# Performance work log

Measured on AMD Instinct MI355X. Metric: run time of the kernel, lower is better.

## Reference

```python
import jax, jax.numpy as jnp
import numpy as np

B, T, S, D, H = 8, 512, 512, 512, 8
DH = D // H
EPS = 1e-5


def _ln(x, g, b):
    m = x.mean(-1, keepdims=True)
    v = x.var(-1, keepdims=True)
    return (x - m) / jnp.sqrt(v + EPS) * g + b


def setup_inputs() -> dict:
    key = jax.random.key(0)
    ks = jax.random.split(key, 24)
    w = lambda k, shp: (jax.random.normal(k, shp, jnp.float32) * 0.02)
    causal = jnp.where(jnp.tril(jnp.ones((T, T), bool)), 0.0, -1e9).astype(jnp.float32)
    return {
        "tgt": jax.random.normal(ks[0], (B, T, D), jnp.float32),
        "memory": jax.random.normal(ks[1], (B, S, D), jnp.float32),
        "tgt_mask": causal,
        "gate": jax.random.uniform(ks[2], (T, D), jnp.float32),
        # self-attn params (torch MultiheadAttention packed in_proj layout)
        "sa_in_w": w(ks[3], (3 * D, D)), "sa_in_b": w(ks[4], (3 * D,)),
        "sa_out_w": w(ks[5], (D, D)), "sa_out_b": w(ks[6], (D,)),
        # cross-attn params
        "ca_in_w": w(ks[7], (3 * D, D)), "ca_in_b": w(ks[8], (3 * D,)),
        "ca_out_w": w(ks[9], (D, D)), "ca_out_b": w(ks[10], (D,)),
        # FFN
        "ff1_w": w(ks[11], (4 * D, D)), "ff1_b": w(ks[12], (4 * D,)),
        "ff2_w": w(ks[13], (D, 4 * D)), "ff2_b": w(ks[14], (D,)),
        # layernorms
        "ln1_g": jnp.ones((D,), jnp.float32), "ln1_b": jnp.zeros((D,), jnp.float32),
        "ln2_g": jnp.ones((D,), jnp.float32), "ln2_b": jnp.zeros((D,), jnp.float32),
        "ln3_g": jnp.ones((D,), jnp.float32), "ln3_b": jnp.zeros((D,), jnp.float32),
    }


def reference(tgt, memory, tgt_mask, gate,
              sa_in_w, sa_in_b, sa_out_w, sa_out_b,
              ca_in_w, ca_in_b, ca_out_w, ca_out_b,
              ff1_w, ff1_b, ff2_w, ff2_b,
              ln1_g, ln1_b, ln2_g, ln2_b, ln3_g, ln3_b):
    b, t, d = tgt.shape
    s = memory.shape[1]
    scale = 1.0 / jnp.sqrt(jnp.float32(DH))

    # ---- self attention (standard batched MHA, additive mask) ----
    wq, wk, wv = jnp.split(sa_in_w, 3, axis=0)
    bq, bk, bv = jnp.split(sa_in_b, 3, axis=0)
    q = ((tgt @ wq.T + bq).reshape(b, t, H, DH)) * scale
    k = (tgt @ wk.T + bk).reshape(b, t, H, DH)
    v = (tgt @ wv.T + bv).reshape(b, t, H, DH)
    scores = jnp.einsum('bthd,bshd->bhts', q, k) + tgt_mask  # (B,H,T,T)
    attn = jax.nn.softmax(scores, axis=-1)
    sa = jnp.einsum('bhts,bshd->bthd', attn, v).reshape(b, t, d) @ sa_out_w.T + sa_out_b
    x = _ln(tgt + sa, ln1_g, ln1_b)

    # ---- gated cross attention ----
    # Original: key_{b,t,s} = W_k(gate_t * memory_{b,s}) + b_k materialized as (B*T,S,D).
    # Faithful refactor: distribute W_k, fold (q W_k) with gate into the query side.
    cwq, cwk, cwv = jnp.split(ca_in_w, 3, axis=0)
    cbq, cbk, cbv = jnp.split(ca_in_b, 3, axis=0)
    cq = ((x @ cwq.T + cbq).reshape(b, t, H, DH)) * scale          # (B,T,H,dh)
    wk_h = cwk.reshape(H, DH, d)                                    # (H,dh,D)
    qW = jnp.einsum('bthe,hed->bthd', cq, wk_h)                     # (B,T,H,D)
    cscores = jnp.einsum('bthd,td,bsd->bhts', qW, gate, memory)     # (B,H,T,S)
    bk_h = cbk.reshape(H, DH)
    cscores = cscores + jnp.einsum('bthe,he->bht', cq, bk_h)[..., None]
    cattn = jax.nn.softmax(cscores, axis=-1)
    cv = (memory @ cwv.T + cbv).reshape(b, s, H, DH)
    ca = jnp.einsum('bhts,bshe->bthe', cattn, cv).reshape(b, t, d) @ ca_out_w.T + ca_out_b
    x = _ln(x + ca, ln2_g, ln2_b)

    # ---- FFN ----
    ff = jax.nn.relu(x @ ff1_w.T + ff1_b) @ ff2_w.T + ff2_b
    return _ln(x + ff, ln3_g, ln3_b)
```

## Files before the change

kernel.cpp:

```cpp
#include <hip/hip_runtime.h>
#include <hip/hip_bf16.h>

#define BB 8
#define TT 512
#define SS 512
#define DD 512
#define HH 8

typedef __attribute__((ext_vector_type(8))) short bf16x8;
typedef __attribute__((ext_vector_type(4))) float f32x4;
typedef unsigned short u16;

__device__ __forceinline__ u16 f2b(float f) {
    __hip_bfloat16 h = __float2bfloat16(f);
    return *reinterpret_cast<u16*>(&h);
}
__device__ __forceinline__ float b2f(u16 v) {
    unsigned int u = ((unsigned int)v) << 16;
    return __builtin_bit_cast(float, u);
}
__device__ __forceinline__ void g2lds16(const void* g, void* l) {
    __builtin_amdgcn_global_load_lds(
        (const __attribute__((address_space(1))) void*)g,
        (__attribute__((address_space(3))) void*)l, 16, 0, 0);
}
template <int N> __device__ __forceinline__ void waitvm();
template <> __device__ __forceinline__ void waitvm<0>()  { asm volatile("s_waitcnt vmcnt(0)" ::: "memory"); }
template <> __device__ __forceinline__ void waitvm<4>()  { asm volatile("s_waitcnt vmcnt(4)" ::: "memory"); }
template <> __device__ __forceinline__ void waitvm<6>()  { asm volatile("s_waitcnt vmcnt(6)" ::: "memory"); }
template <> __device__ __forceinline__ void waitvm<8>()  { asm volatile("s_waitcnt vmcnt(8)" ::: "memory"); }
__device__ __forceinline__ void barrier_raw() {
    asm volatile("" ::: "memory");
    __builtin_amdgcn_s_barrier();
    asm volatile("" ::: "memory");
}
__device__ __forceinline__ void xcd_swz(int& bx, int& by, int& bz) {
    const int gx = gridDim.x, gy = gridDim.y, gz = gridDim.z;
    const int n = gx * gy * gz;
    const int flat = bx + gx * (by + gy * bz);
    const int q = n >> 3;
    const int nf = (flat & 7) * q + (flat >> 3);
    bx = nf % gx;
    const int r = nf / gx;
    by = r % gy;
    bz = r / gy;
}

struct CastSegs {
    const float* s[9];
    u16* d[9];
    int cum[10];
    const float* wsrc;
    u16* wdst;
};
__global__ __launch_bounds__(256) void cast_multi(CastSegs sg) {
    const int total = sg.cum[9];
    for (int i = blockIdx.x * 256 + threadIdx.x; i < total; i += gridDim.x * 256) {
        int k = 0;
#pragma unroll
        for (int j = 1; j < 9; ++j) k += (i >= sg.cum[j]);
        const int loc = i - sg.cum[k];
        float4 v = ((const float4*)sg.s[k])[loc];
        ushort4 u;
        u.x = f2b(v.x); u.y = f2b(v.y); u.z = f2b(v.z); u.w = f2b(v.w);
        ((ushort4*)sg.d[k])[loc] = u;
    }
    for (int idx = blockIdx.x * 256 + threadIdx.x; idx < 262144; idx += gridDim.x * 256) {
        const int h = idx >> 15, d = (idx >> 6) & 511, e = idx & 63;
        sg.wdst[idx] = f2b(sg.wsrc[(size_t)(512 + h * 64 + e) * 512 + d]);
    }
}

template <int TM, int TN, bool RELU, bool GATE, typename OutT = u16, bool ADDBIAS = true>
__global__ __launch_bounds__(256) void gemm_bf16(
    const u16* __restrict__ A, int lda, long az,
    const u16* __restrict__ Bw, int ldb, long bz,
    const float* __restrict__ bias, const float* __restrict__ biasB,
    const float* __restrict__ gate,
    OutT* __restrict__ C, int ldo, long cz,
    int K, float alpha, float alphaB) {
    __shared__ __align__(16) u16 As[2][TM * 64];
    __shared__ __align__(16) u16 Bs[2][TN * 64];
    int bx = blockIdx.x, by = blockIdx.y, bzz = blockIdx.z;
    xcd_swz(bx, by, bzz);
    const int tid = threadIdx.x;
    const int wave = tid >> 6, lane = tid & 63;
    const int lm = lane & 15, lg = lane >> 4;
    const int wm = wave >> 1, wn = wave & 1;
    const int m0 = by * TM, n0 = bx * TN;
    A += (size_t)bzz * az;
    Bw += (size_t)bzz * bz;
    C += (size_t)bzz * cz;
    constexpr int MI = TM / 32;
    constexpr int FN = TN / 32;
    constexpr int LPS = MI + FN;

    f32x4 acc[MI][FN];
#pragma unroll
    for (int mi = 0; mi < MI; ++mi)
#pragma unroll
        for (int ni = 0; ni < FN; ++ni) acc[mi][ni] = (f32x4){0.f, 0.f, 0.f, 0.f};

    const int srow = lane >> 3;
    const int sbyte = ((lane & 7) << 4) ^ (srow << 4);
    const int xk = (lm & 7) << 4;

    auto stage = [&](int buf, int kt) {
#pragma unroll
        for (int j = 0; j < MI; ++j) {
            const int r = wave * (TM / 4) + j * 8;
            g2lds16((const char*)(A + (size_t)(m0 + r + srow) * lda + kt) + sbyte,
                    (char*)As[buf] + (size_t)r * 128);
        }
#pragma unroll
        for (int j = 0; j < FN; ++j) {
            const int r = wave * (TN / 4) + j * 8;
            g2lds16((const char*)(Bw + (size_t)(n0 + r + srow) * ldb + kt) + sbyte,
                    (char*)Bs[buf] + (size_t)r * 128);
        }
    };

    stage(0, 0);
    const int NK = K >> 6;
    for (int t = 0; t < NK; ++t) {
        const int cur = t & 1;
        if (t + 1 < NK) { stage(cur ^ 1, (t + 1) << 6); waitvm<LPS>(); }
        else            { waitvm<0>(); }
        barrier_raw();
#pragma unroll
        for (int kh = 0; kh < 2; ++kh) {
            const int cb = kh * 64 + lg * 16;
            bf16x8 af[MI], bfr[FN];
#pragma unroll
            for (int mi = 0; mi < MI; ++mi) {
                const int row = wm * (TM / 2) + mi * 16 + lm;
                af[mi] = *(const bf16x8*)((const char*)As[cur] + row * 128 + (cb ^ xk));
            }
#pragma unroll
            for (int ni = 0; ni < FN; ++ni) {
                const int row = wn * (TN / 2) + ni * 16 + lm;
                bfr[ni] = *(const bf16x8*)((const char*)Bs[cur] + row * 128 + (cb ^ xk));
            }
#pragma unroll
            for (int mi = 0; mi < MI; ++mi)
#pragma unroll
                for (int ni = 0; ni < FN; ++ni)
                    acc[mi][ni] = __builtin_amdgcn_mfma_f32_16x16x32_bf16(
                        af[mi], bfr[ni], acc[mi][ni], 0, 0, 0);
        }
        barrier_raw();
    }

    const float* bp = bzz ? biasB : bias;
    const float al = bzz ? alphaB : alpha;
#pragma unroll
    for (int mi = 0; mi < MI; ++mi)
#pragma unroll
        for (int ni = 0; ni < FN; ++ni)
#pragma unroll
            for (int r = 0; r < 4; ++r) {
                const int m = m0 + wm * (TM / 2) + mi * 16 + lg * 4 + r;
                const int n = n0 + wn * (TN / 2) + ni * 16 + lm;
                float v = acc[mi][ni][r];
                if constexpr (GATE) v *= gate[(size_t)(m & 511) * 512 + n];
                else if constexpr (ADDBIAS) v = (v + bp[n]) * al;
                if constexpr (RELU) v = fmaxf(v, 0.f);
                if constexpr (sizeof(OutT) == 2) C[(size_t)m * ldo + n] = (OutT)f2b(v);
                else                             C[(size_t)m * ldo + n] = v;
            }
}

__global__ __launch_bounds__(256) void gemm_scores(
    const u16* __restrict__ QWp, const u16* __restrict__ membp,
    u16* __restrict__ SC) {
    __shared__ __align__(16) u16 As[2][128 * 64];
    __shared__ __align__(16) u16 Bs[2][64 * 64];
    int bx = blockIdx.x, by = blockIdx.y, bzz = blockIdx.z;
    xcd_swz(bx, by, bzz);
    const int tid = threadIdx.x;
    const int wave = tid >> 6, lane = tid & 63;
    const int lm = lane & 15, lg = lane >> 4;
    const int wm = wave >> 1, wn = wave & 1;
    const int m0 = by * 128, n0 = bx * 64;
    const int z = bzz, b = z >> 3, h = z & 7;
    const u16* A  = QWp + (size_t)b * TT * 4096 + h * 512;
    const u16* Bw = membp + (size_t)b * SS * 512;
    u16* C = SC + ((size_t)z << 18);

    f32x4 acc[4][2];
#pragma unroll
    for (int mi = 0; mi < 4; ++mi)
#pragma unroll
        for (int ni = 0; ni < 2; ++ni) acc[mi][ni] = (f32x4){0.f, 0.f, 0.f, 0.f};

    const int srow = lane >> 3;
    const int sbyte = ((lane & 7) << 4) ^ (srow << 4);
    const int xk = (lm & 7) << 4;

    auto stage = [&](int buf, int kt) {
#pragma unroll
        for (int j = 0; j < 4; ++j) {
            const int r = wave * 32 + j * 8;
            g2lds16((const char*)(A + (size_t)(m0 + r + srow) * 4096 + kt) + sbyte,
                    (char*)As[buf] + (size_t)r * 128);
        }
#pragma unroll
        for (int j = 0; j < 2; ++j) {
            const int r = wave * 16 + j * 8;
            g2lds16((const char*)(Bw + (size_t)(n0 + r + srow) * 512 + kt) + sbyte,
                    (char*)Bs[buf] + (size_t)r * 128);
        }
    };

    stage(0, 0);
    for (int t = 0; t < 8; ++t) {
        const int cur = t & 1;
        if (t + 1 < 8) { stage(cur ^ 1, (t + 1) << 6); waitvm<6>(); }
        else           { waitvm<0>(); }
        barrier_raw();
#pragma unroll
        for (int kh = 0; kh < 2; ++kh) {
            const int cb = kh * 64 + lg * 16;
            bf16x8 af[4], bfr[2];
#pragma unroll
            for (int mi = 0; mi < 4; ++mi) {
                const int row = wm * 64 + mi * 16 + lm;
                af[mi] = *(const bf16x8*)((const char*)As[cur] + row * 128 + (cb ^ xk));
            }
#pragma unroll
            for (int ni = 0; ni < 2; ++ni) {
                const int row = wn * 32 + ni * 16 + lm;
                bfr[ni] = *(const bf16x8*)((const char*)Bs[cur] + row * 128 + (cb ^ xk));
            }
#pragma unroll
            for (int mi = 0; mi < 4; ++mi)
#pragma unroll
                for (int ni = 0; ni < 2; ++ni)
                    acc[mi][ni] = __builtin_amdgcn_mfma_f32_16x16x32_bf16(
                        af[mi], bfr[ni], acc[mi][ni], 0, 0, 0);
        }
        barrier_raw();
    }
#pragma unroll
    for (int mi = 0; mi < 4; ++mi)
#pragma unroll
        for (int ni = 0; ni < 2; ++ni)
#pragma unroll
            for (int r = 0; r < 4; ++r) {
                const int m = m0 + wm * 64 + mi * 16 + lg * 4 + r;
                const int n = n0 + wn * 32 + ni * 16 + lm;
                C[(size_t)m * 512 + n] = f2b(acc[mi][ni][r]);
            }
}

__global__ __launch_bounds__(256) void softmax_pv(
    const u16* __restrict__ SC, const u16* __restrict__ CV,
    u16* __restrict__ out) {
    int btx = blockIdx.x, bh = blockIdx.y, bb = blockIdx.z;
    xcd_swz(btx, bh, bb);
    const int t0 = btx * 64, h = bh, b = bb;
    const int tid = threadIdx.x, wave = tid >> 6, lane = tid & 63;
    const int lm = lane & 15, lg = lane >> 4;
    __shared__ __align__(16) u16 Vt[64 * 512];

    {
        const int sp = tid * 2;
#pragma unroll
        for (int c = 0; c < 8; ++c) {
            bf16x8 v0 = *(const bf16x8*)(CV + ((size_t)b * SS + sp) * 512 + h * 64 + c * 8);
            bf16x8 v1 = *(const bf16x8*)(CV + ((size_t)b * SS + sp + 1) * 512 + h * 64 + c * 8);
#pragma unroll
            for (int j = 0; j < 8; ++j) {
                const int d = c * 8 + j;
                const unsigned int pk = (unsigned int)(u16)v0[j] |
                                        ((unsigned int)(u16)v1[j] << 16);
                *(unsigned int*)((char*)Vt + ((d << 10) + ((sp * 2) ^ ((d & 7) << 4)))) = pk;
            }
        }
    }

    const int tw = t0 + wave * 16;
    const u16* srow = SC + ((size_t)(b * 8 + h) << 18) + (size_t)(tw + lm) * 512 + lg * 8;
    float sa[16][8];
#pragma unroll
    for (int k = 0; k < 16; ++k) {
        const bf16x8 sv = *(const bf16x8*)(srow + k * 32);
#pragma unroll
        for (int j = 0; j < 8; ++j) sa[k][j] = b2f((u16)sv[j]);
    }
    float mx = -3e38f;
#pragma unroll
    for (int k = 0; k < 16; ++k)
#pragma unroll
        for (int j = 0; j < 8; ++j) mx = fmaxf(mx, sa[k][j]);
    mx = fmaxf(mx, __shfl_xor(mx, 16));
    mx = fmaxf(mx, __shfl_xor(mx, 32));
    float sum = 0.f;
    bf16x8 pb[16];
#pragma unroll
    for (int k = 0; k < 16; ++k) {
#pragma unroll
        for (int j = 0; j < 8; ++j) {
            const float p = __expf(sa[k][j] - mx);
            sum += p;
            pb[k][j] = (short)f2b(p);
        }
    }
    sum += __shfl_xor(sum, 16);
    sum += __shfl_xor(sum, 32);

    __syncthreads();

    f32x4 o[4];
#pragma unroll
    for (int nt = 0; nt < 4; ++nt) o[nt] = (f32x4){0.f, 0.f, 0.f, 0.f};
#pragma unroll
    for (int k = 0; k < 16; ++k) {
#pragma unroll
        for (int nt = 0; nt < 4; ++nt) {
            const int d = nt * 16 + lm;
            const bf16x8 vf = *(const bf16x8*)((const char*)Vt +
                ((d << 10) + ((k * 64 + lg * 16) ^ ((d & 7) << 4))));
            o[nt] = __builtin_amdgcn_mfma_f32_16x16x32_bf16(pb[k], vf, o[nt], 0, 0, 0);
        }
    }
#pragma unroll
    for (int r = 0; r < 4; ++r) {
        const float rs = __shfl(sum, lg * 4 + r);
        const float inv = 1.f / rs;
#pragma unroll
        for (int nt = 0; nt < 4; ++nt)
            out[(size_t)(b * TT + tw + lg * 4 + r) * DD + h * 64 + nt * 16 + lm] =
                f2b(o[nt][r] * inv);
    }
}

__global__ __launch_bounds__(256) void flash_self(const u16* __restrict__ QKV,
                                                  u16* __restrict__ out) {
    int btx = blockIdx.x, bh = blockIdx.y, bb = blockIdx.z;
    xcd_swz(btx, bh, bb);
    const int t0 = btx * 64, h = bh, b = bb;
    const int tid = threadIdx.x, wave = tid >> 6, lane = tid & 63;
    const int lm = lane & 15, lg = lane >> 4;
    __shared__ __align__(16) u16 Ks[32 * 64];
    __shared__ __align__(16) u16 Vt[64][40];
    __shared__ __align__(16) u16 P[4][16][40];

    const int tw = t0 + wave * 16;
    const size_t qrow = (size_t)(b * TT + tw + lm) * 1536 + h * 64;
    bf16x8 qf[2];
    qf[0] = *(const bf16x8*)(QKV + qrow + lg * 8);
    qf[1] = *(const bf16x8*)(QKV + qrow + 32 + lg * 8);

    float m_run[4], l_run[4];
    f32x4 oacc[4];
#pragma unroll
    for (int r = 0; r < 4; ++r) { m_run[r] = -3e38f; l_run[r] = 0.f; }
#pragma unroll
    for (int nt = 0; nt < 4; ++nt) oacc[nt] = (f32x4){0.f, 0.f, 0.f, 0.f};

    const int srow = lane >> 3, sbyte = ((lane & 7) << 4) ^ (srow << 4);
    const int xk = (lm & 7) << 4;
    const int smax = t0 + 64;
    for (int s0 = 0; s0 < smax; s0 += 32) {
        if (s0) __syncthreads();
        g2lds16((const char*)(QKV + (size_t)(b * TT + s0 + wave * 8 + srow) * 1536 +
                              512 + h * 64) + sbyte,
                (char*)Ks + wave * 1024);
        {
            const int s = tid & 31, d0 = (tid >> 5) * 8;
            bf16x8 vv = *(const bf16x8*)(QKV + (size_t)(b * TT + s0 + s) * 1536 +
                                         1024 + h * 64 + d0);
#pragma unroll
            for (int j = 0; j < 8; ++j) Vt[d0 + j][s] = (u16)vv[j];
        }
        __syncthreads();
        if (s0 <= tw + 15) {
            f32x4 sc0 = (f32x4){0.f, 0.f, 0.f, 0.f};
            f32x4 sc1 = (f32x4){0.f, 0.f, 0.f, 0.f};
#pragma unroll
            for (int f = 0; f < 2; ++f) {
                const int cb = f * 64 + lg * 16;
                bf16x8 k0 = *(const bf16x8*)((const char*)Ks + lm * 128 + (cb ^ xk));
                bf16x8 k1 = *(const bf16x8*)((const char*)Ks + (16 + lm) * 128 + (cb ^ xk));
                sc0 = __builtin_amdgcn_mfma_f32_16x16x32_bf16(qf[f], k0, sc0, 0, 0, 0);
                sc1 = __builtin_amdgcn_mfma_f32_16x16x32_bf16(qf[f], k1, sc1, 0, 0, 0);
            }
            float sv0[4], sv1[4], tm[4];
#pragma unroll
            for (int r = 0; r < 4; ++r) {
                const int t = tw + lg * 4 + r;
                sv0[r] = sc0[r] * 0.125f + ((s0 + lm) <= t ? 0.f : -1e9f);
                sv1[r] = sc1[r] * 0.125f + ((s0 + 16 + lm) <= t ? 0.f : -1e9f);
                tm[r] = fmaxf(sv0[r], sv1[r]);
            }
#pragma unroll
            for (int off = 1; off < 16; off <<= 1)
#pragma unroll
                for (int r = 0; r < 4; ++r) tm[r] = fmaxf(tm[r], __shfl_xor(tm[r], off));
            float fac[4], rs[4];
#pragma unroll
            for (int r = 0; r < 4; ++r) {
                const float mn = fmaxf(m_run[r], tm[r]);
                fac[r] = __expf(m_run[r] - mn);
                m_run[r] = mn;
                const float p0 = __expf(sv0[r] - mn);
                const float p1 = __expf(sv1[r] - mn);
                P[wave][lg * 4 + r][lm] = f2b(p0);
                P[wave][lg * 4 + r][16 + lm] = f2b(p1);
                rs[r] = p0 + p1;
            }
#pragma unroll
            for (int off = 1; off < 16; off <<= 1)
#pragma unroll
                for (int r = 0; r < 4; ++r) rs[r] += __shfl_xor(rs[r], off);
#pragma unroll
            for (int r = 0; r < 4; ++r) l_run[r] = l_run[r] * fac[r] + rs[r];
#pragma unroll
            for (int nt = 0; nt < 4; ++nt)
#pragma unroll
                for (int r = 0; r < 4; ++r) oacc[nt][r] *= fac[r];
            const bf16x8 pf = *(const bf16x8*)&P[wave][lm][lg * 8];
#pragma unroll
            for (int nt = 0; nt < 4; ++nt) {
                const bf16x8 vf = *(const bf16x8*)&Vt[nt * 16 + lm][lg * 8];
                oacc[nt] = __builtin_amdgcn_mfma_f32_16x16x32_bf16(pf, vf, oacc[nt], 0, 0, 0);
            }
        }
    }
#pragma unroll
    for (int nt = 0; nt < 4; ++nt)
#pragma unroll
        for (int r = 0; r < 4; ++r)
            out[(size_t)(b * TT + tw + lg * 4 + r) * DD + h * 64 + nt * 16 + lm] =
                f2b(oacc[nt][r] / l_run[r]);
}

template <bool R1B>
__global__ __launch_bounds__(256) void add_ln(
    const void* __restrict__ R1v, const u16* __restrict__ R2,
    const float* __restrict__ g, const float* __restrict__ bta,
    float* __restrict__ outf, u16* __restrict__ outb) {
    const int row = blockIdx.x, tid = threadIdx.x;
    float x0, x1;
    if constexpr (R1B) {
        ushort2 a = ((const ushort2*)((const u16*)R1v + (size_t)row * DD))[tid];
        x0 = b2f(a.x); x1 = b2f(a.y);
    } else {
        float2 a = ((const float2*)((const float*)R1v + (size_t)row * DD))[tid];
        x0 = a.x; x1 = a.y;
    }
    ushort2 c = ((const ushort2*)(R2 + (size_t)row * DD))[tid];
    x0 += b2f(c.x); x1 += b2f(c.y);

    __shared__ float2 red[256];
    red[tid] = make_float2(x0 + x1, x0 * x0 + x1 * x1);
    __syncthreads();
#pragma unroll
    for (int o = 128; o > 0; o >>= 1) {
        if (tid < o) {
            red[tid].x += red[tid + o].x;
            red[tid].y += red[tid + o].y;
        }
        __syncthreads();
    }
    const float mean = red[0].x * (1.f / 512.f);
    const float var = red[0].y * (1.f / 512.f) - mean * mean;
    const float rstd = rsqrtf(var + 1e-5f);
    const int i = tid * 2;
    const float y0 = (x0 - mean) * rstd * g[i] + bta[i];
    const float y1 = (x1 - mean) * rstd * g[i + 1] + bta[i + 1];
    if (outf) ((float2*)(outf + (size_t)row * DD))[tid] = make_float2(y0, y1);
    if (outb) {
        ushort2 ub; ub.x = f2b(y0); ub.y = f2b(y1);
        ((ushort2*)(outb + (size_t)row * DD))[tid] = ub;
    }
}

__global__ __launch_bounds__(256) void add_ln_sk(
    const u16* __restrict__ X2, const float* __restrict__ P0,
    const float* __restrict__ P1, const float* __restrict__ fb,
    const float* __restrict__ g, const float* __restrict__ bta,
    float* __restrict__ outf) {
    const int row = blockIdx.x, tid = threadIdx.x;
    ushort2 a = ((const ushort2*)(X2 + (size_t)row * DD))[tid];
    float2 p0 = ((const float2*)(P0 + (size_t)row * DD))[tid];
    float2 p1 = ((const float2*)(P1 + (size_t)row * DD))[tid];
    const int i = tid * 2;
    float x0 = b2f(a.x) + p0.x + p1.x + fb[i];
    float x1 = b2f(a.y) + p0.y + p1.y + fb[i + 1];

    __shared__ float2 red[256];
    red[tid] = make_float2(x0 + x1, x0 * x0 + x1 * x1);
    __syncthreads();
#pragma unroll
    for (int o = 128; o > 0; o >>= 1) {
        if (tid < o) {
            red[tid].x += red[tid + o].x;
            red[tid].y += red[tid + o].y;
        }
        __syncthreads();
    }
    const float mean = red[0].x * (1.f / 512.f);
    const float var = red[0].y * (1.f / 512.f) - mean * mean;
    const float rstd = rsqrtf(var + 1e-5f);
    const float y0 = (x0 - mean) * rstd * g[i] + bta[i];
    const float y1 = (x1 - mean) * rstd * g[i + 1] + bta[i + 1];
    ((float2*)(outf + (size_t)row * DD))[tid] = make_float2(y0, y1);
}

extern "C" void kernel_launch(void* const* d_in, const int* in_sizes, int n_in,
                              void* d_out, int out_size, void* d_ws, size_t ws_size,
                              hipStream_t stream) {
    const float* tgt      = (const float*)d_in[0];
    const float* memory   = (const float*)d_in[1];
    const float* gate     = (const float*)d_in[3];
    const float* sa_in_w  = (const float*)d_in[4];
    const float* sa_in_b  = (const float*)d_in[5];
    const float* sa_out_w = (const float*)d_in[6];
    const float* sa_out_b = (const float*)d_in[7];
    const float* ca_in_w  = (const float*)d_in[8];
    const float* ca_in_b  = (const float*)d_in[9];
    const float* ca_out_w = (const float*)d_in[10];
    const float* ca_out_b = (const float*)d_in[11];
    const float* ff1_w    = (const float*)d_in[12];
    const float* ff1_b    = (const float*)d_in[13];
    const float* ff2_w    = (const float*)d_in[14];
    const float* ff2_b    = (const float*)d_in[15];
    const float* ln1_g    = (const float*)d_in[16];
    const float* ln1_b    = (const float*)d_in[17];
    const float* ln2_g    = (const float*)d_in[18];
    const float* ln2_b    = (const float*)d_in[19];
    const float* ln3_g    = (const float*)d_in[20];
    const float* ln3_b    = (const float*)d_in[21];

    u16* ws16     = (u16*)d_ws;
    u16* QKVb     = ws16;
    u16* sa_preb  = ws16 + 6291456;
    u16* PRJb     = ws16 + 8388608;
    u16* X1b      = ws16 + 10485760;
    u16* memb     = ws16 + 12582912;
    u16* CQb      = ws16 + 14680064;
    u16* CVb      = ws16 + 16777216;
    u16* QW       = ws16 + 18874368;
    u16* ca_preb  = ws16 + 35651584;
    u16* PRJ2b    = ws16 + 37748736;
    u16* X2b      = ws16 + 39845888;
    u16* HHb      = ws16 + 41943040;
    u16* Wreg     = ws16 + 52428800;
    u16* sa_in_wb = Wreg;
    u16* sa_out_wb= Wreg + 786432;
    u16* ca_wq_b  = Wreg + 1048576;
    u16* ca_wv_b  = Wreg + 1310720;
    u16* WkT      = Wreg + 1572864;
    u16* ca_out_wb= Wreg + 1835008;
    u16* ff1_wb   = Wreg + 2097152;
    u16* ff2_wb   = Wreg + 3145728;
    u16* tgtb     = ws16 + 56623104;
    u16* SCb      = ws16 + 58720256;
    float* FP     = (float*)SCb;
    float* outf   = (float*)d_out;

    const dim3 blk(256);

    CastSegs sg;
    sg.s[0]=tgt; sg.s[1]=memory; sg.s[2]=sa_in_w; sg.s[3]=sa_out_w;
    sg.s[4]=ca_in_w; sg.s[5]=ca_in_w + (size_t)1024*512; sg.s[6]=ca_out_w;
    sg.s[7]=ff1_w; sg.s[8]=ff2_w;
    sg.d[0]=tgtb; sg.d[1]=memb; sg.d[2]=sa_in_wb; sg.d[3]=sa_out_wb;
    sg.d[4]=ca_wq_b; sg.d[5]=ca_wv_b; sg.d[6]=ca_out_wb;
    sg.d[7]=ff1_wb; sg.d[8]=ff2_wb;
    sg.wsrc = ca_in_w; sg.wdst = WkT;
    {
        const int n4[9] = {524288,524288,196608,65536,65536,65536,65536,262144,262144};
        int c = 0;
        for (int i = 0; i < 9; ++i) { sg.cum[i] = c; c += n4[i]; }
        sg.cum[9] = c;
    }
    cast_multi<<<2048, blk, 0, stream>>>(sg);

    gemm_bf16<128,64,false,false><<<dim3(24,32,1), blk, 0, stream>>>(
        tgtb,512,0, sa_in_wb,512,0, sa_in_b,sa_in_b,nullptr,
        QKVb,1536,0, 512, 1.f,1.f);
    flash_self<<<dim3(8,8,8), blk, 0, stream>>>(QKVb, sa_preb);
    gemm_bf16<64,64,false,false><<<dim3(8,64,1), blk, 0, stream>>>(
        sa_preb,512,0, sa_out_wb,512,0, sa_out_b,sa_out_b,nullptr,
        PRJb,512,0, 512, 1.f,1.f);
    add_ln<false><<<4096, blk, 0, stream>>>(tgt, PRJb, ln1_g, ln1_b, nullptr, X1b);
    gemm_bf16<64,64,false,false><<<dim3(8,64,2), blk, 0, stream>>>(
        X1b,512,2097152, ca_wq_b,512,262144, ca_in_b, ca_in_b+1024, nullptr,
        CQb,512,2097152, 512, 0.125f, 1.f);
    gemm_bf16<64,64,false,true><<<dim3(8,64,8), blk, 0, stream>>>(
        CQb,512,64, WkT,64,32768, nullptr,nullptr,gate,
        QW,4096,512, 64, 1.f,1.f);
    gemm_scores<<<dim3(8,4,64), blk, 0, stream>>>(QW, memb, SCb);
    softmax_pv<<<dim3(8,8,8), blk, 0, stream>>>(SCb, CVb, ca_preb);
    gemm_bf16<64,64,false,false><<<dim3(8,64,1), blk, 0, stream>>>(
        ca_preb,512,0, ca_out_wb,512,0, ca_out_b,ca_out_b,nullptr,
        PRJ2b,512,0, 512, 1.f,1.f);
    add_ln<true><<<4096, blk, 0, stream>>>(X1b, PRJ2b, ln2_g, ln2_b, nullptr, X2b);
    gemm_bf16<128,64,true,false><<<dim3(32,32,1), blk, 0, stream>>>(
        X2b,512,0, ff1_wb,512,0, ff1_b,ff1_b,nullptr,
        HHb,2048,0, 512, 1.f,1.f);
    gemm_bf16<64,64,false,false,float,false><<<dim3(8,64,2), blk, 0, stream>>>(
        HHb,2048,1024, ff2_wb,2048,1024, nullptr,nullptr,nullptr,
        FP,512,2097152, 1024, 1.f,1.f);
    add_ln_sk<<<4096, blk, 0, stream>>>(X2b, FP, FP + 2097152, ff2_b,
                                        ln3_g, ln3_b, outf);

    (void)in_sizes; (void)n_in; (void)out_size; (void)ws_size;
}
```

Before: 183.0 us.

## Fuse gated query-key projection into cross-attention score kernel via LDS

```diff
diff --git a/kernel.cpp b/kernel.cpp
--- a/kernel.cpp
+++ b/kernel.cpp
@@ -170,87 +170,108 @@
             }
 }
 
-__global__ __launch_bounds__(256) void gemm_scores(
-    const u16* __restrict__ QWp, const u16* __restrict__ membp,
+__global__ __launch_bounds__(256) void qwg_scores(
+    const u16* __restrict__ CQ, const u16* __restrict__ WkT,
+    const float* __restrict__ gate, const u16* __restrict__ memb,
     u16* __restrict__ SC) {
-    __shared__ __align__(16) u16 As[2][128 * 64];
-    __shared__ __align__(16) u16 Bs[2][64 * 64];
-    int bx = blockIdx.x, by = blockIdx.y, bzz = blockIdx.z;
-    xcd_swz(bx, by, bzz);
-    const int tid = threadIdx.x;
-    const int wave = tid >> 6, lane = tid & 63;
+    int btx = blockIdx.x, bh = blockIdx.y, bb = blockIdx.z;
+    xcd_swz(btx, bh, bb);
+    const int t0 = btx * 64, h = bh, b = bb;
+    const int tid = threadIdx.x, wave = tid >> 6, lane = tid & 63;
     const int lm = lane & 15, lg = lane >> 4;
-    const int wm = wave >> 1, wn = wave & 1;
-    const int m0 = by * 128, n0 = bx * 64;
-    const int z = bzz, b = z >> 3, h = z & 7;
-    const u16* A  = QWp + (size_t)b * TT * 4096 + h * 512;
-    const u16* Bw = membp + (size_t)b * SS * 512;
-    u16* C = SC + ((size_t)z << 18);
-
-    f32x4 acc[4][2];
-#pragma unroll
-    for (int mi = 0; mi < 4; ++mi)
-#pragma unroll
-        for (int ni = 0; ni < 2; ++ni) acc[mi][ni] = (f32x4){0.f, 0.f, 0.f, 0.f};
-
-    const int srow = lane >> 3;
-    const int sbyte = ((lane & 7) << 4) ^ (srow << 4);
-    const int xk = (lm & 7) << 4;
-
-    auto stage = [&](int buf, int kt) {
-#pragma unroll
-        for (int j = 0; j < 4; ++j) {
-            const int r = wave * 32 + j * 8;
-            g2lds16((const char*)(A + (size_t)(m0 + r + srow) * 4096 + kt) + sbyte,
-                    (char*)As[buf] + (size_t)r * 128);
-        }
-#pragma unroll
-        for (int j = 0; j < 2; ++j) {
-            const int r = wave * 16 + j * 8;
-            g2lds16((const char*)(Bw + (size_t)(n0 + r + srow) * 512 + kt) + sbyte,
-                    (char*)Bs[buf] + (size_t)r * 128);
-        }
-    };
-
-    stage(0, 0);
-    for (int t = 0; t < 8; ++t) {
-        const int cur = t & 1;
-        if (t + 1 < 8) { stage(cur ^ 1, (t + 1) << 6); waitvm<6>(); }
-        else           { waitvm<0>(); }
-        barrier_raw();
-#pragma unroll
-        for (int kh = 0; kh < 2; ++kh) {
-            const int cb = kh * 64 + lg * 16;
-            bf16x8 af[4], bfr[2];
-#pragma unroll
-            for (int mi = 0; mi < 4; ++mi) {
-                const int row = wm * 64 + mi * 16 + lm;
-                af[mi] = *(const bf16x8*)((const char*)As[cur] + row * 128 + (cb ^ xk));
-            }
-#pragma unroll
-            for (int ni = 0; ni < 2; ++ni) {
-                const int row = wn * 32 + ni * 16 + lm;
-                bfr[ni] = *(const bf16x8*)((const char*)Bs[cur] + row * 128 + (cb ^ xk));
-            }
+    __shared__ __align__(16) u16 qWg[64 * 512];
+
+    {
+        const int d0 = wave * 128;
+        bf16x8 aq[4][2], wk[8][2];
+#pragma unroll
+        for (int mi = 0; mi < 4; ++mi)
+#pragma unroll
+            for (int kh = 0; kh < 2; ++kh)
+                aq[mi][kh] = *(const bf16x8*)(CQ +
+                    (size_t)(b * TT + t0 + mi * 16 + lm) * 512 + h * 64 + kh * 32 + lg * 8);
+#pragma unroll
+        for (int ni = 0; ni < 8; ++ni)
+#pragma unroll
+            for (int kh = 0; kh < 2; ++kh)
+                wk[ni][kh] = *(const bf16x8*)(WkT + ((size_t)h << 15) +
+                    (size_t)(d0 + ni * 16 + lm) * 64 + kh * 32 + lg * 8);
+        f32x4 acc[4][8];
+#pragma unroll
+        for (int mi = 0; mi < 4; ++mi)
+#pragma unroll
+            for (int ni = 0; ni < 8; ++ni) acc[mi][ni] = (f32x4){0.f, 0.f, 0.f, 0.f};
+#pragma unroll
+        for (int kh = 0; kh < 2; ++kh)
 #pragma unroll
             for (int mi = 0; mi < 4; ++mi)
 #pragma unroll
-                for (int ni = 0; ni < 2; ++ni)
+                for (int ni = 0; ni < 8; ++ni)
                     acc[mi][ni] = __builtin_amdgcn_mfma_f32_16x16x32_bf16(
-                        af[mi], bfr[ni], acc[mi][ni], 0, 0, 0);
-        }
-        barrier_raw();
-    }
-#pragma unroll
-    for (int mi = 0; mi < 4; ++mi)
-#pragma unroll
-        for (int ni = 0; ni < 2; ++ni)
-#pragma unroll
-            for (int r = 0; r < 4; ++r) {
-                const int m = m0 + wm * 64 + mi * 16 + lg * 4 + r;
-                const int n = n0 + wn * 32 + ni * 16 + lm;
-                C[(size_t)m * 512 + n] = f2b(acc[mi][ni][r]);
-            }
+                        aq[mi][kh], wk[ni][kh], acc[mi][ni], 0, 0, 0);
+#pragma unroll
+        for (int mi = 0; mi < 4; ++mi)
+#pragma unroll
+            for (int ni = 0; ni < 8; ++ni)
+#pragma unroll
+                for (int r = 0; r < 4; ++r) {
+                    const int lt = mi * 16 + lg * 4 + r;
+                    const int d = d0 + ni * 16 + lm;
+                    const float v = acc[mi][ni][r] *
+                                    gate[(size_t)(t0 + lt) * 512 + d];
+                    *(u16*)((char*)qWg + lt * 1024 + ((d * 2) ^ ((lt & 7) << 4))) = f2b(v);
+                }
+    }
+    __syncthreads();
+
+    {
+        const int s0 = wave * 128;
+        const int xk = (lm & 7) << 4;
+        f32x4 acc[4][8];
+#pragma unroll
+        for (int mi = 0; mi < 4; ++mi)
+#pragma unroll
+            for (int ni = 0; ni < 8; ++ni) acc[mi][ni] = (f32x4){0.f, 0.f, 0.f, 0.f};
+#pragma unroll
+        for (int kt = 0; kt < 8; ++kt) {
+            bf16x8 a2[4][2];
+#pragma unroll
+            for (int mi = 0; mi < 4; ++mi)
+#pragma unroll
+                for (int kh = 0; kh < 2; ++kh) {
+                    const int row = mi * 16 + lm;
+                    const int cb = kt * 128 + kh * 64 + lg * 16;
+                    a2[mi][kh] = *(const bf16x8*)((const char*)qWg +
+                        row * 1024 + (cb ^ xk));
+                }
+#pragma unroll
+            for (int ni = 0; ni < 8; ++ni) {
+                bf16x8 b2[2];
+#pragma unroll
+                for (int kh = 0; kh < 2; ++kh)
+                    b2[kh] = *(const bf16x8*)(memb +
+                        (size_t)(b * SS + s0 + ni * 16 + lm) * 512 +
+                        kt * 64 + kh * 32 + lg * 8);
+#pragma unroll
+                for (int kh = 0; kh < 2; ++kh)
+#pragma unroll
+                    for (int mi = 0; mi < 4; ++mi)
+                        acc[mi][ni] = __builtin_amdgcn_mfma_f32_16x16x32_bf16(
+                            a2[mi][kh], b2[kh], acc[mi][ni], 0, 0, 0);
+            }
+        }
+        u16* C = SC + ((size_t)(b * 8 + h) << 18);
+#pragma unroll
+        for (int mi = 0; mi < 4; ++mi)
+#pragma unroll
+            for (int ni = 0; ni < 8; ++ni)
+#pragma unroll
+                for (int r = 0; r < 4; ++r) {
+                    const int t = t0 + mi * 16 + lg * 4 + r;
+                    const int s = s0 + ni * 16 + lm;
+                    C[(size_t)t * 512 + s] = f2b(acc[mi][ni][r]);
+                }
+    }
 }
 
 __global__ __launch_bounds__(256) void softmax_pv(
@@ -542,7 +563,6 @@
     u16* memb     = ws16 + 12582912;
     u16* CQb      = ws16 + 14680064;
     u16* CVb      = ws16 + 16777216;
-    u16* QW       = ws16 + 18874368;
     u16* ca_preb  = ws16 + 35651584;
     u16* PRJ2b    = ws16 + 37748736;
     u16* X2b      = ws16 + 39845888;
@@ -590,10 +610,7 @@
     gemm_bf16<64,64,false,false><<<dim3(8,64,2), blk, 0, stream>>>(
         X1b,512,2097152, ca_wq_b,512,262144, ca_in_b, ca_in_b+1024, nullptr,
         CQb,512,2097152, 512, 0.125f, 1.f);
-    gemm_bf16<64,64,false,true><<<dim3(8,64,8), blk, 0, stream>>>(
-        CQb,512,64, WkT,64,32768, nullptr,nullptr,gate,
-        QW,4096,512, 64, 1.f,1.f);
-    gemm_scores<<<dim3(8,4,64), blk, 0, stream>>>(QW, memb, SCb);
+    qwg_scores<<<dim3(8,8,8), blk, 0, stream>>>(CQb, WkT, gate, memb, SCb);
     softmax_pv<<<dim3(8,8,8), blk, 0, stream>>>(SCb, CVb, ca_preb);
     gemm_bf16<64,64,false,false><<<dim3(8,64,1), blk, 0, stream>>>(
         ca_preb,512,0, ca_out_wb,512,0, ca_out_b,ca_out_b,nullptr,
```

Result: slower. 229.8 us (+25.5%).
